# Optimization experiments

Measured on AMD Instinct MI355X. Metric: run time of the kernel, lower is better.

## Reference

```python
import jax, jax.numpy as jnp
import numpy as np

B, T, C, H = 16, 2048, 512, 4
DH = C // H  # head dim = 128


def setup_inputs() -> dict:
    key = jax.random.key(0)
    ks = jax.random.split(key, 12)
    s = 1.0 / np.sqrt(C).astype(np.float32)
    u = lambda k, shape: jax.random.uniform(k, shape, jnp.float32, -s, s)
    return {
        "x": jax.random.normal(ks[0], (B, C, 2, T), jnp.float32),
        "device_embedding": jax.random.normal(ks[1], (1, 2, C), jnp.float32),
        "in_proj_w": u(ks[2], (3 * C, C)),
        "in_proj_b": jnp.zeros((3 * C,), jnp.float32),
        "out_proj_w": u(ks[3], (C, C)),
        "out_proj_b": jnp.zeros((C,), jnp.float32),
        "phone_w": u(ks[4], (C, C)),
        "phone_b": u(ks[5], (C,)),
        "imu_w": u(ks[6], (C, C)),
        "imu_b": u(ks[7], (C,)),
        "output_w": u(ks[8], (C, 2 * C)),
        "output_b": u(ks[9], (C,)),
    }


def reference(x, device_embedding, in_proj_w, in_proj_b, out_proj_w, out_proj_b,
              phone_w, phone_b, imu_w, imu_b, output_w, output_b):
    Bx, Cx, Hdev, Tx = x.shape  # Hdev == 2 devices (phone, IMU)
    N = Bx * Tx
    # (B, C, 2, T) -> (B*T, 2, C), add learned device embedding
    xe = jnp.transpose(x, (0, 3, 2, 1)).reshape(N, 2, Cx) + device_embedding
    # torch nn.MultiheadAttention: packed in_proj, scale 1/sqrt(head_dim)
    wq, wk, wv = jnp.split(in_proj_w, 3, axis=0)
    bq, bk, bv = jnp.split(in_proj_b, 3, axis=0)
    to_heads = lambda t: t.reshape(N, 2, H, DH).transpose(0, 2, 1, 3)  # (N, H, 2, DH)
    q = to_heads(xe @ wq.T + bq)
    k = to_heads(xe @ wk.T + bk)
    v = to_heads(xe @ wv.T + bv)
    scores = jnp.einsum('nhqd,nhkd->nhqk', q, k) / jnp.float32(np.sqrt(DH))
    probs = jax.nn.softmax(scores, axis=-1)  # (N, H, 2, 2)
    ctx = jnp.einsum('nhqk,nhkd->nhqd', probs, v).transpose(0, 2, 1, 3).reshape(N, 2, Cx)
    attended = (ctx @ out_proj_w.T + out_proj_b).reshape(Bx, Tx, 2, Cx)
    phone = attended[:, :, 0, :] @ phone_w.T + phone_b
    imu = attended[:, :, 1, :] @ imu_w.T + imu_b
    out = jnp.concatenate([phone, imu], axis=-1) @ output_w.T + output_b  # (B, T, C)
    out = jnp.transpose(out, (0, 2, 1))  # (B, C, T)
    # head-averaged attention weights, then averaged over time
    avg_attention = probs.mean(axis=1).reshape(Bx, Tx, 2, 2).mean(axis=1)  # (B, 2, 2)
    return out, avg_attention
```

## Files before the change

kernel.cpp:

```cpp
#include <hip/hip_runtime.h>
#include <stdint.h>

typedef unsigned short u16;
typedef short short8 __attribute__((ext_vector_type(8)));
typedef float floatx4 __attribute__((ext_vector_type(4)));

__device__ __forceinline__ u16 f2bf(float f) {
  union { float f; unsigned u; } t; t.f = f;
  return (u16)((t.u + 0x7fffu + ((t.u >> 16) & 1u)) >> 16);
}
__device__ __forceinline__ float lo16(unsigned w) { union { unsigned u; float f; } t; t.u = w << 16; return t.f; }
__device__ __forceinline__ float hi16(unsigned w) { union { unsigned u; float f; } t; t.u = w & 0xffff0000u; return t.f; }
__device__ __forceinline__ void unpack8(uint4 v, float* f) {
  f[0]=lo16(v.x); f[1]=hi16(v.x); f[2]=lo16(v.y); f[3]=hi16(v.y);
  f[4]=lo16(v.z); f[5]=hi16(v.z); f[6]=lo16(v.w); f[7]=hi16(v.w);
}
__device__ __forceinline__ uint4 pack8(const u16* o) {
  uint4 v;
  v.x = (unsigned)o[0] | ((unsigned)o[1] << 16);
  v.y = (unsigned)o[2] | ((unsigned)o[3] << 16);
  v.z = (unsigned)o[4] | ((unsigned)o[5] << 16);
  v.w = (unsigned)o[6] | ((unsigned)o[7] << 16);
  return v;
}

__device__ __forceinline__ void gll16(const void* g, void* l) {
  __builtin_amdgcn_global_load_lds(
      (const __attribute__((address_space(1))) void*)(uintptr_t)(g),
      (__attribute__((address_space(3))) void*)(unsigned)(uintptr_t)(l),
      16, 0, 0);
}

__device__ __forceinline__ void cvt4(const float* s, u16* d, int g) {
  float4 v = *(const float4*)(s + (size_t)g * 4);
  ushort4 o; o.x = f2bf(v.x); o.y = f2bf(v.y); o.z = f2bf(v.z); o.w = f2bf(v.w);
  *(ushort4*)(d + (size_t)g * 4) = o;
}
__global__ __launch_bounds__(256)
void prep_convert(const float* __restrict__ inw, const float* __restrict__ phw,
                  const float* __restrict__ imw, const float* __restrict__ ow,
                  const float* __restrict__ outw,
                  u16* __restrict__ inw_bf, u16* __restrict__ phw_bf,
                  u16* __restrict__ imw_bf, u16* __restrict__ ow_bf,
                  u16* __restrict__ outwT) {
  int which = blockIdx.y;
  int g = blockIdx.x * 256 + threadIdx.x;
  if (which == 0) { if (g < 196608) cvt4(inw, inw_bf, g); }
  else if (which == 1) { if (g < 65536) cvt4(phw, phw_bf, g); }
  else if (which == 2) { if (g < 65536) cvt4(imw, imw_bf, g); }
  else if (which == 3) { if (g < 131072) cvt4(ow, ow_bf, g); }
  else {
    if (g < 65536) {
      int i0 = (g >> 9) * 4, j = g & 511;
      ushort4 o;
      o.x = f2bf(outw[(size_t)(i0 + 0) * 512 + j]);
      o.y = f2bf(outw[(size_t)(i0 + 1) * 512 + j]);
      o.z = f2bf(outw[(size_t)(i0 + 2) * 512 + j]);
      o.w = f2bf(outw[(size_t)(i0 + 3) * 512 + j]);
      outwT[(size_t)j * 512 + i0 + 0] = o.x;
      outwT[(size_t)j * 512 + i0 + 1] = o.y;
      outwT[(size_t)j * 512 + i0 + 2] = o.z;
      outwT[(size_t)j * 512 + i0 + 3] = o.w;
    }
  }
}

__global__ __launch_bounds__(256)
void uv_kernel(const float* __restrict__ phw, const float* __restrict__ phb,
               const float* __restrict__ imw, const float* __restrict__ imb,
               const float* __restrict__ outb, float* __restrict__ uv) {
  int g = blockIdx.x * 256 + threadIdx.x;
  int i = g & 511;
  const float* W = (g < 512) ? phw : imw;
  const float* bb = (g < 512) ? phb : imb;
  float s = bb[i];
#pragma unroll 4
  for (int c = 0; c < 512; ++c) s += W[(size_t)i * 512 + c] * outb[c];
  uv[g] = s;
}

__global__ __launch_bounds__(256)
void bcomb_kernel(const float* __restrict__ ow, const float* __restrict__ ob,
                  const float* __restrict__ uv, float* __restrict__ bcomb) {
  int i = blockIdx.x * 256 + threadIdx.x;
  float s = ob[i];
#pragma unroll 4
  for (int r = 0; r < 1024; ++r) s += ow[(size_t)i * 1024 + r] * uv[r];
  bcomb[i] = s;
}

__global__ __launch_bounds__(256)
void build_xe(const float* __restrict__ x, const float* __restrict__ emb,
              u16* __restrict__ xe) {
  __shared__ u16 tile[64][66];
  int bt = blockIdx.x;
  int tt = bt & 31, ct = (bt >> 5) & 7, d = (bt >> 8) & 1, b = bt >> 9;
  int t0 = tt * 64, c0 = ct * 64;
  int tid = threadIdx.x;
  int q = tid & 15, r = tid >> 4;
#pragma unroll
  for (int p = 0; p < 4; ++p) {
    int c = p * 16 + r;
    const float* src = x + ((size_t)((b * 512 + c0 + c) * 2 + d)) * 2048 + t0 + q * 4;
    float4 v = *(const float4*)src;
    float e = emb[d * 512 + c0 + c];
    ushort4 o; o.x = f2bf(v.x + e); o.y = f2bf(v.y + e); o.z = f2bf(v.z + e); o.w = f2bf(v.w + e);
    *(ushort4*)&tile[c][q * 4] = o;
  }
  __syncthreads();
  int cq = tid & 7, tp = tid >> 3;
  int cc0 = cq * 8;
  u16 o0[8], o1[8];
#pragma unroll
  for (int i = 0; i < 8; ++i) {
    unsigned w2 = *(const unsigned*)&tile[cc0 + i][2 * tp];
    o0[i] = (u16)(w2 & 0xffffu); o1[i] = (u16)(w2 >> 16);
  }
  size_t n = (size_t)b * 2048 + t0 + 2 * tp;
  *(uint4*)(xe + (n * 2 + d) * 512 + c0 + cc0) = pack8(o0);
  *(uint4*)(xe + ((n + 1) * 2 + d) * 512 + c0 + cc0) = pack8(o1);
}

template<int EPI>
__global__ __launch_bounds__(256, 3)
void gemm_bt(const u16* __restrict__ A, int lda,
             const u16* __restrict__ B, int ldb,
             const float* __restrict__ bias,
             void* __restrict__ Cv, int ldc, int K,
             const float* __restrict__ P) {
  __shared__ u16 As[128 * 64];
  __shared__ u16 Bs[128 * 64];
  int m0 = blockIdx.x * 128;
  int n0 = blockIdx.y * 128;
  int t = threadIdx.x;
  int lane = t & 63;
  int w = t >> 6;
  int wm = (w >> 1) * 64, wn = (w & 1) * 64;
  int l15 = lane & 15, quad = lane >> 4;

  floatx4 acc[4][4];
#pragma unroll
  for (int i = 0; i < 4; ++i)
#pragma unroll
    for (int j = 0; j < 4; ++j) acc[i][j] = (floatx4){0.f, 0.f, 0.f, 0.f};

  int lrow = lane >> 3, lcol = (lane & 7) * 8;
  const u16* gA = A + (size_t)(m0 + w * 32 + lrow) * lda + lcol;
  const u16* gB = B + (size_t)(n0 + w * 32 + lrow) * ldb + lcol;
  u16* lA = As + (w * 32) * 64;
  u16* lB = Bs + (w * 32) * 64;

  int KT = K >> 6;
  for (int kt = 0; kt < KT; ++kt) {
    int ko = kt * 64;
#pragma unroll
    for (int j = 0; j < 4; ++j) {
      gll16(gA + (size_t)(j * 8) * lda + ko, lA + (j * 8) * 64);
      gll16(gB + (size_t)(j * 8) * ldb + ko, lB + (j * 8) * 64);
    }
    __syncthreads();
#pragma unroll
    for (int ki = 0; ki < 2; ++ki) {
      short8 af[4], bfv[4];
#pragma unroll
      for (int i = 0; i < 4; ++i)
        af[i] = *(const short8*)&As[(wm + i * 16 + l15) * 64 + ki * 32 + quad * 8];
#pragma unroll
      for (int j = 0; j < 4; ++j)
        bfv[j] = *(const short8*)&Bs[(wn + j * 16 + l15) * 64 + ki * 32 + quad * 8];
#pragma unroll
      for (int i = 0; i < 4; ++i)
#pragma unroll
        for (int j = 0; j < 4; ++j)
          acc[i][j] = __builtin_amdgcn_mfma_f32_16x16x32_bf16(af[i], bfv[j], acc[i][j], 0, 0, 0);
    }
    __syncthreads();
  }

#pragma unroll
  for (int i = 0; i < 4; ++i) {
    int mrow = m0 + wm + i * 16 + quad * 4;
    float4 P0, P1;
    if (EPI == 2) {
      int np0 = mrow >> 1;
      P0 = *(const float4*)&P[((size_t)np0 * 4 + blockIdx.y) * 4];
      P1 = *(const float4*)&P[((size_t)(np0 + 1) * 4 + blockIdx.y) * 4];
    }
#pragma unroll
    for (int j = 0; j < 4; ++j) {
      int col = n0 + wn + j * 16 + l15;
      float bv = bias[col];
      floatx4 a = acc[i][j];
      if (EPI == 1) {
        int bb = mrow >> 11, ti = mrow & 2047;
        float4 o; o.x = a[0] + bv; o.y = a[1] + bv; o.z = a[2] + bv; o.w = a[3] + bv;
        *(float4*)&((float*)Cv)[((size_t)bb * ldc + col) * 2048 + ti] = o;
      } else if (EPI == 2) {
        float a0 = a[0] + bv, a1 = a[1] + bv, a2 = a[2] + bv, a3 = a[3] + bv;
        u16* C = (u16*)Cv;
        C[(size_t)(mrow + 0) * ldc + col] = f2bf(P0.x * a0 + P0.y * a1);
        C[(size_t)(mrow + 1) * ldc + col] = f2bf(P0.z * a0 + P0.w * a1);
        C[(size_t)(mrow + 2) * ldc + col] = f2bf(P1.x * a2 + P1.y * a3);
        C[(size_t)(mrow + 3) * ldc + col] = f2bf(P1.z * a2 + P1.w * a3);
      } else {
        u16* C = (u16*)Cv;
#pragma unroll
        for (int r = 0; r < 4; ++r)
          C[(size_t)(mrow + r) * ldc + col] = f2bf(a[r] + bv);
      }
    }
  }
}

__global__ __launch_bounds__(256)
void score_kernel(const u16* __restrict__ QK, float* __restrict__ P,
                  float* __restrict__ asum) {
  int g = blockIdx.x * 256 + threadIdx.x;
  int n = g >> 2, h = g & 3;
  const u16* q0 = QK + (size_t)(2 * n) * 1024 + h * 128;
  const u16* q1 = q0 + 1024;
  const u16* k0 = q0 + 512;
  const u16* k1 = k0 + 1024;

  float s00 = 0.f, s01 = 0.f, s10 = 0.f, s11 = 0.f;
#pragma unroll
  for (int c = 0; c < 128; c += 8) {
    float fq0[8], fq1[8], fk0[8], fk1[8];
    unpack8(*(const uint4*)(q0 + c), fq0);
    unpack8(*(const uint4*)(q1 + c), fq1);
    unpack8(*(const uint4*)(k0 + c), fk0);
    unpack8(*(const uint4*)(k1 + c), fk1);
#pragma unroll
    for (int u = 0; u < 8; ++u) {
      s00 += fq0[u] * fk0[u]; s01 += fq0[u] * fk1[u];
      s10 += fq1[u] * fk0[u]; s11 += fq1[u] * fk1[u];
    }
  }
  const float sc = 0.08838834764831845f;
  s00 *= sc; s01 *= sc; s10 *= sc; s11 *= sc;
  float m0v = fmaxf(s00, s01), m1v = fmaxf(s10, s11);
  float e00 = __expf(s00 - m0v), e01 = __expf(s01 - m0v);
  float e10 = __expf(s10 - m1v), e11 = __expf(s11 - m1v);
  float i0 = 1.f / (e00 + e01), i1 = 1.f / (e10 + e11);
  float4 p; p.x = e00 * i0; p.y = e01 * i0; p.z = e10 * i1; p.w = e11 * i1;
  *(float4*)&P[(size_t)g * 4] = p;

  float pv[4] = {p.x, p.y, p.z, p.w};
#pragma unroll
  for (int k2 = 0; k2 < 4; ++k2) {
    float v = pv[k2];
    v += __shfl_down(v, 32, 64); v += __shfl_down(v, 16, 64);
    v += __shfl_down(v, 8, 64);  v += __shfl_down(v, 4, 64);
    v += __shfl_down(v, 2, 64);  v += __shfl_down(v, 1, 64);
    pv[k2] = v;
  }
  __shared__ float red[4][4];
  int lane = threadIdx.x & 63, wv = threadIdx.x >> 6;
  if (lane == 0) { red[wv][0] = pv[0]; red[wv][1] = pv[1]; red[wv][2] = pv[2]; red[wv][3] = pv[3]; }
  __syncthreads();
  if (threadIdx.x < 4) {
    float s = red[0][threadIdx.x] + red[1][threadIdx.x] + red[2][threadIdx.x] + red[3][threadIdx.x];
    int b = (blockIdx.x * 64) >> 11;
    atomicAdd(&asum[b * 4 + threadIdx.x], s);
  }
}

__global__ void avg_kernel(const float* __restrict__ asum, float* __restrict__ out) {
  int i = threadIdx.x;
  out[16777216 + i] = asum[i] * (1.0f / 8192.0f);
}

extern "C" void kernel_launch(void* const* d_in, const int* in_sizes, int n_in,
                              void* d_out, int out_size, void* d_ws, size_t ws_size,
                              hipStream_t stream) {
  const float* x    = (const float*)d_in[0];
  const float* emb  = (const float*)d_in[1];
  const float* inw  = (const float*)d_in[2];
  const float* inb  = (const float*)d_in[3];
  const float* outw = (const float*)d_in[4];
  const float* outb = (const float*)d_in[5];
  const float* phw  = (const float*)d_in[6];
  const float* phb  = (const float*)d_in[7];
  const float* imw  = (const float*)d_in[8];
  const float* imb  = (const float*)d_in[9];
  const float* ow   = (const float*)d_in[10];
  const float* ob   = (const float*)d_in[11];
  float* outF = (float*)d_out;

  char* wsb = (char*)d_ws;
  u16*   ctx    = (u16*)wsb;
  u16*   QK     = (u16*)(wsb + 67108864);
  u16*   outwT  = (u16*)(wsb + 67108864);
  u16*   phw_bf = (u16*)(wsb + 67633152);
  u16*   imw_bf = (u16*)(wsb + 68157440);
  u16*   ow_bf  = (u16*)(wsb + 68681728);
  u16*   T1T    = (u16*)(wsb + 69730304);
  u16*   T2T    = (u16*)(wsb + 70254592);
  u16*   inw_bf = (u16*)(wsb + 201326592);
  u16*   Wcomb  = (u16*)(wsb + 202899456);
  float* uv     = (float*)(wsb + 203948032);
  float* bcomb  = (float*)(wsb + 203952128);
  float* P      = (float*)(wsb + 203954176);
  float* asum   = (float*)(wsb + 206051328);
  float* zbias  = (float*)(wsb + 206051584);
  u16*   xe     = (u16*)d_out;

  hipMemsetAsync(asum, 0, 2304, stream);

  build_xe<<<8192, 256, 0, stream>>>(x, emb, xe);

  prep_convert<<<dim3(768, 5), 256, 0, stream>>>(inw, phw, imw, ow, outw,
                                                 inw_bf, phw_bf, imw_bf, ow_bf, outwT);
  gemm_bt<0><<<dim3(4, 4), 256, 0, stream>>>(outwT, 512, phw_bf, 512, zbias, T1T, 512, 512, nullptr);
  gemm_bt<0><<<dim3(4, 4), 256, 0, stream>>>(outwT, 512, imw_bf, 512, zbias, T2T, 512, 512, nullptr);
  gemm_bt<0><<<dim3(4, 4), 256, 0, stream>>>(ow_bf, 1024, T1T, 512, zbias, Wcomb, 1024, 512, nullptr);
  gemm_bt<0><<<dim3(4, 4), 256, 0, stream>>>(ow_bf + 512, 1024, T2T, 512, zbias, Wcomb + 512, 1024, 512, nullptr);
  uv_kernel<<<4, 256, 0, stream>>>(phw, phb, imw, imb, outb, uv);
  bcomb_kernel<<<2, 256, 0, stream>>>(ow, ob, uv, bcomb);

  gemm_bt<0><<<dim3(512, 8), 256, 0, stream>>>(xe, 512, inw_bf, 512, inb,
                                               QK, 1024, 512, nullptr);
  score_kernel<<<512, 256, 0, stream>>>(QK, P, asum);
  gemm_bt<2><<<dim3(512, 4), 256, 0, stream>>>(xe, 512, inw_bf + 524288, 512,
                                               inb + 1024, ctx, 512, 512, P);
  gemm_bt<1><<<dim3(256, 4), 256, 0, stream>>>(ctx, 1024, Wcomb, 1024,
                                               bcomb, outF, 512, 1024, nullptr);
  avg_kernel<<<1, 64, 0, stream>>>(asum, outF);
}
```

Baseline: 655.2 us.

## Replace main GEMMs with 256x256-tile 512-thread kernel and 4-stage LDS pipeline

Adds a gemm256 kernel that computes 256x256 output tiles with 8 waves. Operands are loaded straight from global memory into LDS through a 4-deep ring buffer, with explicit vmcnt waits and barriers. MFMA priority is raised during compute, and block IDs are remapped so that adjacent blocks spread across XCDs. The three large GEMMs (QK projection, V projection with the softmax-mix epilogue, and the combined output projection) now use it, aiming for more data reuse per tile and better latency hiding. The cost is a large LDS footprint (128KB) and register pressure. Fewer blocks are launched (256 for the last GEMM), which may leave CUs underused.

New measurement: 623.6 us. -4.8%, faster.

```diff
diff --git a/kernel.cpp b/kernel.cpp
--- a/kernel.cpp
+++ b/kernel.cpp
@@ -212,6 +212,122 @@
   }
 }
 
+__device__ __forceinline__ void compute_tile(const u16 (&Asr)[4][8192],
+                                             const u16 (&Bsr)[4][8192],
+                                             int bo, int aoff, int boff,
+                                             floatx4 (&acc)[8][4]) {
+  short8 af[8], bfv[4];
+#pragma unroll
+  for (int i = 0; i < 8; ++i)
+    af[i] = *(const short8*)&Asr[bo][aoff + i * 512];
+#pragma unroll
+  for (int j = 0; j < 4; ++j)
+    bfv[j] = *(const short8*)&Bsr[bo][boff + j * 512];
+  __builtin_amdgcn_s_setprio(1);
+#pragma unroll
+  for (int i = 0; i < 8; ++i)
+#pragma unroll
+    for (int j = 0; j < 4; ++j)
+      acc[i][j] = __builtin_amdgcn_mfma_f32_16x16x32_bf16(af[i], bfv[j], acc[i][j], 0, 0, 0);
+  __builtin_amdgcn_s_setprio(0);
+}
+
+template<int EPI>
+__global__ __launch_bounds__(512, 2)
+void gemm256(const u16* __restrict__ A, int lda,
+             const u16* __restrict__ B, int ldb,
+             const float* __restrict__ bias,
+             void* __restrict__ Cv, int ldc, int K,
+             const float* __restrict__ P, int nbs) {
+  __shared__ u16 As[4][8192];
+  __shared__ u16 Bs[4][8192];
+  int nwg = gridDim.x;
+  int bid = blockIdx.x;
+  int chunk = nwg >> 3;
+  int g = (bid & 7) * chunk + (bid >> 3);
+  int nb = g & ((1 << nbs) - 1), mb = g >> nbs;
+  int m0 = mb * 256, n0 = nb * 256;
+  int t = threadIdx.x;
+  int lane = t & 63, w = t >> 6;
+  int wr = w >> 2, wc = w & 3;
+  int l15 = lane & 15, quad = lane >> 4;
+  int wb = w * 512;
+  int srow = t >> 2, sch = (t & 3) * 8;
+  const u16* gA0 = A + (size_t)(m0 + srow) * lda + sch;
+  const u16* gA1 = gA0 + (size_t)128 * lda;
+  const u16* gB0 = B + (size_t)(n0 + srow) * ldb + sch;
+  const u16* gB1 = gB0 + (size_t)128 * ldb;
+
+  floatx4 acc[8][4];
+#pragma unroll
+  for (int i = 0; i < 8; ++i)
+#pragma unroll
+    for (int j = 0; j < 4; ++j) acc[i][j] = (floatx4){0.f, 0.f, 0.f, 0.f};
+
+  int aoff = (wr * 128 + l15) * 32 + quad * 8;
+  int boff = (wc * 64 + l15) * 32 + quad * 8;
+  int KT = K >> 5;
+
+#define STAGE256(ts) { int _b = (ts) & 3; int _ko = (ts) * 32;             \
+    gll16(gA0 + _ko, (void*)&As[_b][wb]);                                  \
+    gll16(gA1 + _ko, (void*)&As[_b][wb + 4096]);                           \
+    gll16(gB0 + _ko, (void*)&Bs[_b][wb]);                                  \
+    gll16(gB1 + _ko, (void*)&Bs[_b][wb + 4096]); }
+
+  STAGE256(0)
+  STAGE256(1)
+  STAGE256(2)
+  for (int tt = 0; tt < KT - 3; ++tt) {
+    STAGE256(tt + 3)
+    asm volatile("s_waitcnt vmcnt(12)" ::: "memory");
+    asm volatile("s_barrier" ::: "memory");
+    compute_tile(As, Bs, tt & 3, aoff, boff, acc);
+    asm volatile("s_barrier" ::: "memory");
+  }
+  asm volatile("s_waitcnt vmcnt(8)" ::: "memory");
+  asm volatile("s_barrier" ::: "memory");
+  compute_tile(As, Bs, (KT - 3) & 3, aoff, boff, acc);
+  asm volatile("s_waitcnt vmcnt(4)" ::: "memory");
+  asm volatile("s_barrier" ::: "memory");
+  compute_tile(As, Bs, (KT - 2) & 3, aoff, boff, acc);
+  asm volatile("s_waitcnt vmcnt(0)" ::: "memory");
+  asm volatile("s_barrier" ::: "memory");
+  compute_tile(As, Bs, (KT - 1) & 3, aoff, boff, acc);
+#undef STAGE256
+
+#pragma unroll
+  for (int i = 0; i < 8; ++i) {
+    int mrow = m0 + wr * 128 + i * 16 + quad * 4;
+#pragma unroll
+    for (int j = 0; j < 4; ++j) {
+      int col = n0 + wc * 64 + j * 16 + l15;
+      float bv = bias[col];
+      floatx4 a = acc[i][j];
+      if (EPI == 1) {
+        int bb = mrow >> 11, ti = mrow & 2047;
+        float4 o; o.x = a[0] + bv; o.y = a[1] + bv; o.z = a[2] + bv; o.w = a[3] + bv;
+        *(float4*)&((float*)Cv)[((size_t)bb * ldc + col) * 2048 + ti] = o;
+      } else if (EPI == 2) {
+        int np0 = mrow >> 1;
+        int h = col >> 7;
+        float4 P0 = *(const float4*)&P[((size_t)np0 * 4 + h) * 4];
+        float4 P1 = *(const float4*)&P[((size_t)(np0 + 1) * 4 + h) * 4];
+        float a0 = a[0] + bv, a1 = a[1] + bv, a2 = a[2] + bv, a3 = a[3] + bv;
+        u16* C = (u16*)Cv;
+        C[(size_t)(mrow + 0) * ldc + col] = f2bf(P0.x * a0 + P0.y * a1);
+        C[(size_t)(mrow + 1) * ldc + col] = f2bf(P0.z * a0 + P0.w * a1);
+        C[(size_t)(mrow + 2) * ldc + col] = f2bf(P1.x * a2 + P1.y * a3);
+        C[(size_t)(mrow + 3) * ldc + col] = f2bf(P1.z * a2 + P1.w * a3);
+      } else {
+        u16* C = (u16*)Cv;
+#pragma unroll
+        for (int r = 0; r < 4; ++r)
+          C[(size_t)(mrow + r) * ldc + col] = f2bf(a[r] + bv);
+      }
+    }
+  }
+}
+
 __global__ __launch_bounds__(256)
 void score_kernel(const u16* __restrict__ QK, float* __restrict__ P,
                   float* __restrict__ asum) {
@@ -318,12 +434,12 @@
   uv_kernel<<<4, 256, 0, stream>>>(phw, phb, imw, imb, outb, uv);
   bcomb_kernel<<<2, 256, 0, stream>>>(ow, ob, uv, bcomb);
 
-  gemm_bt<0><<<dim3(512, 8), 256, 0, stream>>>(xe, 512, inw_bf, 512, inb,
-                                               QK, 1024, 512, nullptr);
+  gemm256<0><<<1024, 512, 0, stream>>>(xe, 512, inw_bf, 512, inb,
+                                       QK, 1024, 512, nullptr, 2);
   score_kernel<<<512, 256, 0, stream>>>(QK, P, asum);
-  gemm_bt<2><<<dim3(512, 4), 256, 0, stream>>>(xe, 512, inw_bf + 524288, 512,
-                                               inb + 1024, ctx, 512, 512, P);
-  gemm_bt<1><<<dim3(256, 4), 256, 0, stream>>>(ctx, 1024, Wcomb, 1024,
-                                               bcomb, outF, 512, 1024, nullptr);
+  gemm256<2><<<512, 512, 0, stream>>>(xe, 512, inw_bf + 524288, 512,
+                                      inb + 1024, ctx, 512, 512, P, 1);
+  gemm256<1><<<256, 512, 0, stream>>>(ctx, 1024, Wcomb, 1024,
+                                      bcomb, outF, 512, 1024, nullptr, 1);
   avg_kernel<<<1, 64, 0, stream>>>(asum, outF);
 }
```
